# Performance work log

Measured on AMD Instinct MI355X. Metric: run time of the kernel, lower is better.

## Reference

```python
import jax, jax.numpy as jnp
import numpy as np
from functools import partial

C = 10   # number of regular-repr fields
G = 4    # C4 rotation group order
EPS = 1e-5


def _lift_kernel(w):
    """Lifting (trivial->regular) P4 kernel. w: [C, Cin, k, k] ->
    full kernel [C*G, Cin, k, k] with output channel layout (field, orientation)."""
    ks = [jnp.rot90(w, r, axes=(-2, -1)) for r in range(G)]  # each [C,Cin,k,k]
    k = jnp.stack(ks, axis=1)                                 # [C,G,Cin,k,k]
    return k.reshape(w.shape[0] * G, w.shape[1], w.shape[2], w.shape[3])


def _gconv_kernel(w):
    """Regular->regular P4 kernel. w: [Cout, Cin, G, k, k] (indexed by relative
    input orientation) -> full kernel [Cout*G, Cin*G, k, k].
    K[co*G+r, ci*G+s] = rot90(w[co, ci, (s-r) mod G], r)."""
    Cout, Cin, _, k1, k2 = w.shape
    ks = []
    for r in range(G):
        wr = jnp.roll(w, shift=r, axis=2)             # wr[..., s, :, :] = w[..., (s-r)%G]
        wr = jnp.rot90(wr, r, axes=(-2, -1))          # rotate spatially by r*90deg
        ks.append(wr)
    k = jnp.stack(ks, axis=1)                          # [Cout, G, Cin, G, k, k]
    return k.reshape(Cout * G, Cin * G, k1, k2)


def _conv(x, k, pad):
    return jax.lax.conv_general_dilated(
        x, k, window_strides=(1, 1), padding=pad,
        dimension_numbers=('NCHW', 'OIHW', 'NCHW'))


def _bn_relu(x, gamma, beta):
    """InnerBatchNorm (stats shared over the G orientations of each field) + ReLU."""
    B, CG, H, W = x.shape
    xr = x.reshape(B, C, G, H, W)
    m = xr.mean(axis=(0, 2, 3, 4), keepdims=True)
    v = xr.var(axis=(0, 2, 3, 4), keepdims=True)
    g = gamma[None, :, None, None, None]
    b = beta[None, :, None, None, None]
    y = (xr - m) * jax.lax.rsqrt(v + EPS) * g + b
    return jnp.maximum(y.reshape(B, CG, H, W), 0.0)


def _maxpool2(x):
    return jax.lax.reduce_window(x, -jnp.inf, jax.lax.max,
                                 (1, 1, 2, 2), (1, 1, 2, 2), 'VALID')


def setup_inputs() -> dict:
    key = jax.random.key(0)
    ks = jax.random.split(key, 20)
    B = 1024
    x = jax.random.normal(ks[0], (B, 1, 28, 28), dtype=jnp.float32)
    w1 = jax.random.normal(ks[1], (C, 1, 3, 3), dtype=jnp.float32) * 0.3
    w2 = jax.random.normal(ks[2], (C, C, G, 3, 3), dtype=jnp.float32) * 0.1
    w3 = jax.random.normal(ks[3], (C, C, G, 3, 3), dtype=jnp.float32) * 0.1
    w4 = jax.random.normal(ks[4], (C, C, G, 3, 3), dtype=jnp.float32) * 0.1
    w5 = jax.random.normal(ks[5], (C, C, G, 3, 3), dtype=jnp.float32) * 0.1
    w6 = jax.random.normal(ks[6], (C, C, G, 3, 3), dtype=jnp.float32) * 0.1
    w7 = jax.random.normal(ks[7], (C, C, G, 4, 4), dtype=jnp.float32) * 0.1
    g1 = jnp.ones((C,), jnp.float32) + 0.1 * jax.random.normal(ks[8], (C,))
    b1 = 0.1 * jax.random.normal(ks[9], (C,))
    g2 = jnp.ones((C,), jnp.float32) + 0.1 * jax.random.normal(ks[10], (C,))
    b2 = 0.1 * jax.random.normal(ks[11], (C,))
    gs = jnp.ones((C,), jnp.float32) + 0.1 * jax.random.normal(ks[12], (C,))
    bs = 0.1 * jax.random.normal(ks[13], (C,))
    wfc = jax.random.normal(ks[14], (10, C * 11 * 11), dtype=jnp.float32) * 0.05
    bfc = jnp.zeros((10,), jnp.float32)
    return dict(x=x, w1=w1, w2=w2, w3=w3, w4=w4, w5=w5, w6=w6, w7=w7,
                g1=g1, b1=b1, g2=g2, b2=b2, gs=gs, bs=bs, wfc=wfc, bfc=bfc)


PAD1 = [(1, 1), (1, 1)]
PAD0 = [(0, 0), (0, 0)]


def reference(x, w1, w2, w3, w4, w5, w6, w7, g1, b1, g2, b2, gs, bs, wfc, bfc):
    # block1: lifting P4 conv 3x3 pad1 + InnerBN + ReLU  -> [B, 40, 28, 28]
    h = _bn_relu(_conv(x, _lift_kernel(w1), PAD1), g1, b1)
    # block2: P4 conv + BN + ReLU + 2x2 max pool         -> [B, 40, 14, 14]
    h = _maxpool2(_bn_relu(_conv(h, _gconv_kernel(w2), PAD1), g2, b2))
    # blocks 3-6: P4 conv + shared BN/ReLU               -> [B, 40, 14, 14]
    for w in (w3, w4, w5, w6):
        h = _bn_relu(_conv(h, _gconv_kernel(w), PAD1), gs, bs)
    # block7: P4 conv 4x4 pad0 + shared BN/ReLU          -> [B, 40, 11, 11]
    h = _bn_relu(_conv(h, _gconv_kernel(w7), PAD0), gs, bs)
    # group pooling: max over the G orientations of each field -> [B, 10, 11, 11]
    B = h.shape[0]
    h = h.reshape(B, C, G, 11, 11).max(axis=2)
    # fc
    return h.reshape(B, -1) @ wfc.T + bfc
```

## Files before the change

### kernel.cpp

```cpp
#include <hip/hip_runtime.h>

#define EPSV 1e-5f
#define INV28 (1.f / 3211264.f)
#define INV14 (1.f / 802816.f)
#define INV11 (1.f / 495616.f)

typedef _Float16 v8h __attribute__((ext_vector_type(8)));
typedef _Float16 v4h __attribute__((ext_vector_type(4)));
typedef _Float16 v2h __attribute__((ext_vector_type(2)));
typedef float v4f __attribute__((ext_vector_type(4)));

__device__ __forceinline__ int h2i(v2h v) { union { v2h h; int i; } u; u.h = v; return u.i; }
__device__ __forceinline__ v2h i2h(int i) { union { v2h h; int i; } u; u.i = i; return u.h; }
__device__ __forceinline__ int pmax2(int a, int b) {
  v2h x = i2h(a), y = i2h(b), r;
  r[0] = x[0] > y[0] ? x[0] : y[0];
  r[1] = x[1] > y[1] ? x[1] : y[1];
  return h2i(r);
}

__device__ __forceinline__ int rotsrc(int r, int dy, int dx, int K) {
  int sy, sx;
  if (r == 0)      { sy = dy;       sx = dx; }
  else if (r == 1) { sy = dx;       sx = K - 1 - dy; }
  else if (r == 2) { sy = K - 1 - dy; sx = K - 1 - dx; }
  else             { sy = K - 1 - dx; sx = dy; }
  return sy * K + sx;
}

__device__ __forceinline__ float gw_val(const float* __restrict__ w, int oc, int g,
                                        int j, int KS) {
  int tap = g / 5, cig = g % 5, ci = cig * 8 + j;
  int co = oc >> 2, r = oc & 3, cin = ci >> 2, s = ci & 3;
  int srel = (s - r) & 3;
  return w[((co * 10 + cin) * 4 + srel) * (KS * KS) + rotsrc(r, tap / KS, tap % KS, KS)];
}

__device__ __forceinline__ float stat8a(const float* __restrict__ p, int i) {
  float v = 0.f;
#pragma unroll
  for (int c = 0; c < 8; ++c)
    v += __hip_atomic_load(&p[c * 32 + i], __ATOMIC_RELAXED, __HIP_MEMORY_SCOPE_AGENT);
  return v;
}

__global__ void prep_kernel(const float* __restrict__ w1, const float* __restrict__ w2,
                            const float* __restrict__ w3, const float* __restrict__ w4,
                            const float* __restrict__ w5, const float* __restrict__ w6,
                            const float* __restrict__ w7,
                            _Float16* __restrict__ K1h, _Float16* __restrict__ Wh,
                            float* __restrict__ stats) {
  int idx = blockIdx.x * blockDim.x + threadIdx.x;
  if (idx < 1792) { stats[idx] = 0.f; return; }
  idx -= 1792;
  if (idx < 1536) {
    int mt = idx >> 9, l = (idx >> 3) & 63, j = idx & 7;
    int m = l & 15, quad = l >> 4;
    int k = quad * 8 + j, oc = mt * 16 + m;
    float val = 0.f;
    if (k < 9 && oc < 40) {
      int c = oc >> 2, r = oc & 3;
      val = w1[c * 9 + rotsrc(r, k / 3, k % 3, 3)];
    }
    K1h[idx] = (_Float16)val;
    return;
  }
  idx -= 1536;
  if (idx < 92160) {
    int l = idx / 18432, r0 = idx % 18432;
    const float* w = (l == 0) ? w2 : (l == 1) ? w3 : (l == 2) ? w4 : (l == 3) ? w5 : w6;
    int mt = r0 / 6144, r1 = r0 % 6144;
    int c = r1 / 512, r2 = r1 % 512;
    int q = r2 / 128, r3 = r2 % 128;
    int ocl = r3 / 8, j = r3 % 8;
    int oc = mt * 16 + ocl, g = c * 4 + q;
    float val = 0.f;
    if (oc < 40 && g < 45) val = gw_val(w, oc, g, j, 3);
    Wh[idx] = (_Float16)val;
    return;
  }
  idx -= 92160;
  if (idx < 30720) {
    int mt = idx / 10240, r1 = idx % 10240;
    int c = r1 / 512, r2 = r1 % 512;
    int q = r2 / 128, r3 = r2 % 128;
    int ocl = r3 / 8, j = r3 % 8;
    int oc = mt * 16 + ocl, g = c * 4 + q;
    float val = 0.f;
    if (oc < 40) val = gw_val(w7, oc, g, j, 4);
    Wh[92160 + idx] = (_Float16)val;
  }
}

__global__ __launch_bounds__(256) void conv1_stats(
    const float* __restrict__ x, const _Float16* __restrict__ K1h,
    float* __restrict__ stats) {
  __shared__ float ximg[900];
  __shared__ float sstat[20];
  const int tid = threadIdx.x, img = blockIdx.x;
  if (tid < 20) sstat[tid] = 0.f;
  for (int i = tid; i < 900; i += 256) {
    int gy = i / 30 - 1, gx = i % 30 - 1;
    ximg[i] = (gy >= 0 && gy < 28 && gx >= 0 && gx < 28)
                  ? x[img * 784 + gy * 28 + gx] : 0.f;
  }
  __syncthreads();
  const int lane = tid & 63, wv = tid >> 6;
  const int m = lane & 15, quad = lane >> 4;
  v8h a1[3];
#pragma unroll
  for (int mt = 0; mt < 3; ++mt)
    a1[mt] = *(const v8h*)(K1h + (mt * 64 + lane) * 8);
  float s[3] = {0.f, 0.f, 0.f}, q[3] = {0.f, 0.f, 0.f};
  for (int st = wv; st < 49; st += 4) {
    const int p = st * 16 + m;
    const int y = p / 28, xx = p % 28;
    v8h b;
#pragma unroll
    for (int j = 0; j < 8; ++j) {
      const int t = quad * 8 + j;
      float v = 0.f;
      if (t < 9) v = ximg[(y + t / 3) * 30 + xx + t % 3];
      b[j] = (_Float16)v;
    }
#pragma unroll
    for (int mt = 0; mt < 3; ++mt) {
      v4f acc = {0.f, 0.f, 0.f, 0.f};
      acc = __builtin_amdgcn_mfma_f32_16x16x32_f16(a1[mt], b, acc, 0, 0, 0);
#pragma unroll
      for (int r = 0; r < 4; ++r) { float v = acc[r]; s[mt] += v; q[mt] += v * v; }
    }
  }
#pragma unroll
  for (int mt = 0; mt < 3; ++mt) {
    float sv = s[mt], qv = q[mt];
#pragma unroll
    for (int off = 1; off <= 8; off <<= 1) {
      sv += __shfl_xor(sv, off, 64);
      qv += __shfl_xor(qv, off, 64);
    }
    if (m == 0 && ((mt < 2) || (quad < 2))) {
      atomicAdd(&sstat[mt * 4 + quad], sv);
      atomicAdd(&sstat[10 + mt * 4 + quad], qv);
    }
  }
  __syncthreads();
  if (tid < 20) atomicAdd(&stats[(img & 7) * 32 + tid], sstat[tid]);
}

template<int R>
__device__ __forceinline__ void band_impl(
    const int img, const int y0,
    const float* __restrict__ x, const _Float16* __restrict__ K1h,
    const _Float16* __restrict__ Wl,
    float* __restrict__ xpatch, _Float16* __restrict__ tile,
    const float* __restrict__ sc, const float* __restrict__ sh,
    float* __restrict__ sstat, _Float16* __restrict__ T0) {
  constexpr int NPIX = R * 28, NSUB = NPIX / 16, NSW = (NSUB + 3) / 4;
  constexpr int SROWS = R + 2, XR = R + 4;
  const int tid = threadIdx.x;
  const int lane = tid & 63, wv = tid >> 6;
  const int m = lane & 15, quad = lane >> 4;

  for (int i = tid; i < XR * 32; i += 256) {
    int gy = y0 - 2 + i / 32, gx = i % 32 - 2;
    xpatch[i] = (gy >= 0 && gy < 28 && gx >= 0 && gx < 28)
                    ? x[(long)img * 784 + gy * 28 + gx] : 0.f;
  }
  __syncthreads();

  {
    v8h a1[3];
#pragma unroll
    for (int mt = 0; mt < 3; ++mt)
      a1[mt] = *(const v8h*)(K1h + (mt * 64 + lane) * 8);
    constexpr int NPIXS = SROWS * 30;
    constexpr int NST = (NPIXS + 15) / 16;
    for (int st = wv; st < NST; st += 4) {
      const int p = st * 16 + m;
      const int pc = p < NPIXS ? p : NPIXS - 1;
      const int iy = pc / 30, ix = pc % 30;
      v8h b;
#pragma unroll
      for (int j = 0; j < 8; ++j) {
        const int t = quad * 8 + j;
        float v = 0.f;
        if (t < 9) v = xpatch[(iy + t / 3) * 32 + ix + t % 3];
        b[j] = (_Float16)v;
      }
      const int gy = y0 + iy - 1, gx = ix - 1;
      const bool wr = p < NPIXS;
      const bool inb = wr && gy >= 0 && gy < 28 && gx >= 0 && gx < 28;
      _Float16* tb = &tile[pc * 40];
#pragma unroll
      for (int mt = 0; mt < 3; ++mt) {
        v4f a = {0.f, 0.f, 0.f, 0.f};
        a = __builtin_amdgcn_mfma_f32_16x16x32_f16(a1[mt], b, a, 0, 0, 0);
        if (((mt < 2) || (quad < 2)) && wr) {
          const int f = mt * 4 + quad;
          const float scf = sc[f], shf = sh[f];
          v4h pk;
#pragma unroll
          for (int r = 0; r < 4; ++r)
            pk[r] = inb ? (_Float16)fmaxf(0.f, fmaf(a[r], scf, shf)) : (_Float16)0.f;
          *(v4h*)(tb + mt * 16 + quad * 4) = pk;
        }
      }
    }
  }
  __syncthreads();

  int pbase[NSW];
  bool sv[NSW];
#pragma unroll
  for (int s = 0; s < NSW; ++s) {
    int ns = wv + 4 * s;
    sv[s] = ns < NSUB;
    int i = (sv[s] ? ns : 0) * 16 + m;
    int q = i >> 2, c2 = i & 3;
    int yy = 2 * (q / 14) + (c2 >> 1), xx = 2 * (q % 14) + (c2 & 1);
    pbase[s] = (yy * 30 + xx) * 40;
  }
  v4f acc[3][NSW] = {};

  const _Float16* wlane = Wl + (quad * 16 + m) * 8;
  for (int c = 0; c < 12; ++c) {
    int g = 4 * c + quad; g = g > 44 ? 44 : g;
    int tap = g / 5, cig = g - tap * 5;
    int boff = ((tap / 3) * 30 + (tap % 3)) * 40 + cig * 8;
    v8h bfr[NSW];
#pragma unroll
    for (int s = 0; s < NSW; ++s)
      if (sv[s]) bfr[s] = *(const v8h*)&tile[pbase[s] + boff];
    v8h afr[3];
#pragma unroll
    for (int mt = 0; mt < 3; ++mt)
      afr[mt] = *(const v8h*)(wlane + (mt * 12 + c) * 512);
#pragma unroll
    for (int s = 0; s < NSW; ++s)
      if (sv[s]) {
#pragma unroll
        for (int mt = 0; mt < 3; ++mt)
          acc[mt][s] = __builtin_amdgcn_mfma_f32_16x16x32_f16(afr[mt], bfr[s],
                                                             acc[mt][s], 0, 0, 0);
      }
  }

#pragma unroll
  for (int mt = 0; mt < 3; ++mt) {
    float svv = 0.f, qvv = 0.f;
#pragma unroll
    for (int s = 0; s < NSW; ++s)
      if (sv[s]) {
#pragma unroll
        for (int r = 0; r < 4; ++r) { float v = acc[mt][s][r]; svv += v; qvv += v * v; }
      }
    const bool ocok = (mt < 2) || (quad < 2);
#pragma unroll
    for (int off = 1; off <= 8; off <<= 1) {
      svv += __shfl_xor(svv, off, 64);
      qvv += __shfl_xor(qvv, off, 64);
    }
    if (m == 0 && ocok) {
      atomicAdd(&sstat[mt * 4 + quad], svv);
      atomicAdd(&sstat[10 + mt * 4 + quad], qvv);
    }
  }

#pragma unroll
  for (int s = 0; s < NSW; ++s) {
    if (!sv[s]) continue;
    const int ns = wv + 4 * s;
    const int q = ns * 4 + (m >> 2);
    const int tb4 = (img * 256 + (y0 / 2 + q / 14 + 1) * 16 + (q % 14 + 1)) * 40;
#pragma unroll
    for (int mt = 0; mt < 3; ++mt) {
      const bool ocok = (mt < 2) || (quad < 2);
      if (!ocok) continue;
      v2h w0, w1;
      w0[0] = (_Float16)acc[mt][s][0]; w0[1] = (_Float16)acc[mt][s][1];
      w1[0] = (_Float16)acc[mt][s][2]; w1[1] = (_Float16)acc[mt][s][3];
      int a0 = h2i(w0), a1 = h2i(w1);
      a0 = pmax2(a0, __shfl_xor(a0, 1, 64));
      a0 = pmax2(a0, __shfl_xor(a0, 2, 64));
      a1 = pmax2(a1, __shfl_xor(a1, 1, 64));
      a1 = pmax2(a1, __shfl_xor(a1, 2, 64));
      if ((m & 3) == 0) {
        v2h r0 = i2h(a0), r1 = i2h(a1);
        v4h o;
        o[0] = r0[0]; o[1] = r0[1]; o[2] = r1[0]; o[3] = r1[1];
        *(v4h*)(T0 + (long)tb4 + mt * 16 + quad * 4) = o;
      }
    }
  }
}

__global__ __launch_bounds__(256) void conv_band_all(
    const float* __restrict__ x, const _Float16* __restrict__ K1h,
    const _Float16* __restrict__ Wl, const float* __restrict__ pstats,
    const float* __restrict__ pgamma, const float* __restrict__ pbeta,
    _Float16* __restrict__ T0, float* __restrict__ stats) {
  __shared__ __attribute__((aligned(16))) _Float16 tile[10 * 30 * 40];
  __shared__ float xpatch[12 * 32];
  __shared__ float sc[10], sh[10], sstat[20];
  const int tid = threadIdx.x;
  if (tid < 20) sstat[tid] = 0.f;
  if (tid >= 32 && tid < 42) {
    int f = tid - 32;
    float mu = stat8a(pstats, f) * INV28, q = stat8a(pstats, 10 + f) * INV28;
    float isd = rsqrtf(q - mu * mu + EPSV);
    float s = pgamma[f] * isd;
    sc[f] = s; sh[f] = pbeta[f] - mu * s;
  }
  const int bid = blockIdx.x;
  int img;
  if (bid < 3072) {
    img = bid / 3;
    band_impl<8>(img, (bid % 3) * 8, x, K1h, Wl, xpatch, tile, sc, sh, sstat, T0);
  } else {
    img = bid - 3072;
    band_impl<4>(img, 24, x, K1h, Wl, xpatch, tile, sc, sh, sstat, T0);
  }
  __syncthreads();
  if (tid < 20) atomicAdd(&stats[(img & 7) * 32 + tid], sstat[tid]);
}

__global__ __launch_bounds__(256) void conv_tile(
    const _Float16* __restrict__ Tin, const _Float16* __restrict__ Wl,
    const float* __restrict__ pstats, const float* __restrict__ pg,
    const float* __restrict__ pb, float pinvn,
    _Float16* __restrict__ Tout, float* __restrict__ stG) {
  __shared__ __attribute__((aligned(16))) _Float16 tile[256 * 40];
  __shared__ v2h scH[10], shH[10];
  __shared__ float sstat[20];
  const int tid = threadIdx.x, img = blockIdx.x;
  const int lane = tid & 63, wv = tid >> 6;
  const int m = lane & 15, quad = lane >> 4;
  if (tid < 20) sstat[tid] = 0.f;
  if (tid >= 32 && tid < 42) {
    int f = tid - 32;
    float mu = stat8a(pstats, f) * pinvn, q = stat8a(pstats, 10 + f) * pinvn;
    float isd = rsqrtf(q - mu * mu + EPSV);
    float s = pg[f] * isd;
    _Float16 sH = (_Float16)s, hH = (_Float16)(pb[f] - mu * s);
    v2h t0, t1;
    t0[0] = sH; t0[1] = sH; t1[0] = hH; t1[1] = hH;
    scH[f] = t0; shH[f] = t1;
  }
  __syncthreads();
  {
    const int iy = tid >> 4, ix = tid & 15;
    const bool border = (iy == 0) | (iy == 15) | (ix == 0) | (ix == 15);
    const _Float16* src = Tin + ((long)img * 256 + tid) * 40;
    _Float16* dst = &tile[tid * 40];
    if (!border) {
#pragma unroll
      for (int cg5 = 0; cg5 < 5; ++cg5) {
        v8h rv = *(const v8h*)(src + cg5 * 8);
        v2h* r2 = (v2h*)&rv;
        v8h pk; v2h* p2 = (v2h*)&pk;
#pragma unroll
        for (int pr = 0; pr < 4; ++pr) {
          const int f = cg5 * 2 + (pr >> 1);
          v2h t = r2[pr] * scH[f] + shH[f];
          v2h o;
          o[0] = t[0] > (_Float16)0.f ? t[0] : (_Float16)0.f;
          o[1] = t[1] > (_Float16)0.f ? t[1] : (_Float16)0.f;
          p2[pr] = o;
        }
        *(v8h*)(dst + cg5 * 8) = pk;
      }
    } else {
      v8h z;
#pragma unroll
      for (int u = 0; u < 8; ++u) z[u] = (_Float16)0.f;
#pragma unroll
      for (int cg5 = 0; cg5 < 5; ++cg5) *(v8h*)(dst + cg5 * 8) = z;
    }
  }
  __syncthreads();

  int pb3[4], n3[4];
  bool sv3[4], va3[4];
#pragma unroll
  for (int s = 0; s < 4; ++s) {
    int ns = wv + 4 * s;
    sv3[s] = ns < 13;
    int n = ns * 16 + m;
    va3[s] = sv3[s] && (n < 196);
    n = n < 196 ? n : 195;
    n3[s] = n;
    pb3[s] = ((n / 14) * 16 + (n % 14)) * 40;
  }
  const int wofs = (quad * 16 + m) * 8;
  v4f acc[3][4];
#pragma unroll
  for (int mt = 0; mt < 3; ++mt)
#pragma unroll
    for (int s = 0; s < 4; ++s) acc[mt][s] = (v4f){0.f, 0.f, 0.f, 0.f};
  for (int c = 0; c < 12; ++c) {
    int g = 4 * c + quad; g = g > 44 ? 44 : g;
    int tap = g / 5, cig = g - tap * 5;
    int boff = ((tap / 3) * 16 + (tap % 3)) * 40 + cig * 8;
    v8h bfr[4];
#pragma unroll
    for (int s = 0; s < 4; ++s)
      if (sv3[s]) bfr[s] = *(const v8h*)&tile[pb3[s] + boff];
    v8h afr[3];
#pragma unroll
    for (int mt = 0; mt < 3; ++mt)
      afr[mt] = *(const v8h*)(Wl + wofs + (mt * 12 + c) * 512);
#pragma unroll
    for (int s = 0; s < 4; ++s)
      if (sv3[s]) {
#pragma unroll
        for (int mt = 0; mt < 3; ++mt)
          acc[mt][s] = __builtin_amdgcn_mfma_f32_16x16x32_f16(afr[mt], bfr[s],
                                                             acc[mt][s], 0, 0, 0);
      }
  }

#pragma unroll
  for (int mt = 0; mt < 3; ++mt) {
    float svv = 0.f, qvv = 0.f;
#pragma unroll
    for (int s = 0; s < 4; ++s)
      if (va3[s]) {
#pragma unroll
        for (int r = 0; r < 4; ++r) { float v = acc[mt][s][r]; svv += v; qvv += v * v; }
      }
    const bool ocok = (mt < 2) || (quad < 2);
#pragma unroll
    for (int off = 1; off <= 8; off <<= 1) {
      svv += __shfl_xor(svv, off, 64);
      qvv += __shfl_xor(qvv, off, 64);
    }
    if (m == 0 && ocok) {
      atomicAdd(&sstat[mt * 4 + quad], svv);
      atomicAdd(&sstat[10 + mt * 4 + quad], qvv);
    }
  }
  __syncthreads();
  if (tid < 20) atomicAdd(&stG[(img & 7) * 32 + tid], sstat[tid]);

#pragma unroll
  for (int mt = 0; mt < 3; ++mt) {
    const bool ocok = (mt < 2) || (quad < 2);
    if (!ocok) continue;
#pragma unroll
    for (int s = 0; s < 4; ++s)
      if (va3[s]) {
        v4h pk;
#pragma unroll
        for (int r = 0; r < 4; ++r) pk[r] = (_Float16)acc[mt][s][r];
        const int n = n3[s];
        *(v4h*)(Tout + ((long)img * 256 + (n / 14 + 1) * 16 + (n % 14 + 1)) * 40
                + mt * 16 + quad * 4) = pk;
      }
  }
}

__global__ __launch_bounds__(256) void conv7_tile(
    const _Float16* __restrict__ Tin, const _Float16* __restrict__ Wl,
    const float* __restrict__ pstats, const float* __restrict__ pg,
    const float* __restrict__ pb,
    _Float16* __restrict__ T7, float* __restrict__ stG) {
  __shared__ __attribute__((aligned(16))) _Float16 tile[256 * 40];
  __shared__ v2h scH[10], shH[10];
  __shared__ float sstat[20];
  const int tid = threadIdx.x, img = blockIdx.x;
  const int lane = tid & 63, wv = tid >> 6;
  const int m = lane & 15, quad = lane >> 4;
  if (tid < 20) sstat[tid] = 0.f;
  if (tid >= 32 && tid < 42) {
    int f = tid - 32;
    float mu = stat8a(pstats, f) * INV14, q = stat8a(pstats, 10 + f) * INV14;
    float isd = rsqrtf(q - mu * mu + EPSV);
    float s = pg[f] * isd;
    _Float16 sH = (_Float16)s, hH = (_Float16)(pb[f] - mu * s);
    v2h t0, t1;
    t0[0] = sH; t0[1] = sH; t1[0] = hH; t1[1] = hH;
    scH[f] = t0; shH[f] = t1;
  }
  __syncthreads();
  {
    const int iy = tid >> 4, ix = tid & 15;
    const bool border = (iy == 0) | (iy == 15) | (ix == 0) | (ix == 15);
    const _Float16* src = Tin + ((long)img * 256 + tid) * 40;
    _Float16* dst = &tile[tid * 40];
    if (!border) {
#pragma unroll
      for (int cg5 = 0; cg5 < 5; ++cg5) {
        v8h rv = *(const v8h*)(src + cg5 * 8);
        v2h* r2 = (v2h*)&rv;
        v8h pk; v2h* p2 = (v2h*)&pk;
#pragma unroll
        for (int pr = 0; pr < 4; ++pr) {
          const int f = cg5 * 2 + (pr >> 1);
          v2h t = r2[pr] * scH[f] + shH[f];
          v2h o;
          o[0] = t[0] > (_Float16)0.f ? t[0] : (_Float16)0.f;
          o[1] = t[1] > (_Float16)0.f ? t[1] : (_Float16)0.f;
          p2[pr] = o;
        }
        *(v8h*)(dst + cg5 * 8) = pk;
      }
    } else {
      v8h z;
#pragma unroll
      for (int u = 0; u < 8; ++u) z[u] = (_Float16)0.f;
#pragma unroll
      for (int cg5 = 0; cg5 < 5; ++cg5) *(v8h*)(dst + cg5 * 8) = z;
    }
  }
  __syncthreads();

  int pb7[2], n7[2];
  bool va7[2];
#pragma unroll
  for (int s = 0; s < 2; ++s) {
    int ns = wv + 4 * s;
    int n = ns * 16 + m;
    va7[s] = n < 121;
    n = n < 121 ? n : 120;
    n7[s] = n;
    pb7[s] = ((n / 11 + 1) * 16 + (n % 11 + 1)) * 40;
  }
  const int wofs = (quad * 16 + m) * 8;
  v4f acc[3][2];
#pragma unroll
  for (int mt = 0; mt < 3; ++mt)
#pragma unroll
    for (int s = 0; s < 2; ++s) acc[mt][s] = (v4f){0.f, 0.f, 0.f, 0.f};
  for (int c = 0; c < 20; ++c) {
    int g = 4 * c + quad;
    int tap = g / 5, cig = g - tap * 5;
    int boff = ((tap >> 2) * 16 + (tap & 3)) * 40 + cig * 8;
    v8h bfr[2];
#pragma unroll
    for (int s = 0; s < 2; ++s) bfr[s] = *(const v8h*)&tile[pb7[s] + boff];
    v8h afr[3];
#pragma unroll
    for (int mt = 0; mt < 3; ++mt)
      afr[mt] = *(const v8h*)(Wl + wofs + (mt * 20 + c) * 512);
#pragma unroll
    for (int s = 0; s < 2; ++s)
#pragma unroll
      for (int mt = 0; mt < 3; ++mt)
        acc[mt][s] = __builtin_amdgcn_mfma_f32_16x16x32_f16(afr[mt], bfr[s],
                                                           acc[mt][s], 0, 0, 0);
  }

#pragma unroll
  for (int mt = 0; mt < 3; ++mt) {
    float svv = 0.f, qvv = 0.f;
#pragma unroll
    for (int s = 0; s < 2; ++s)
      if (va7[s]) {
#pragma unroll
        for (int r = 0; r < 4; ++r) { float v = acc[mt][s][r]; svv += v; qvv += v * v; }
      }
    const bool ocok = (mt < 2) || (quad < 2);
#pragma unroll
    for (int off = 1; off <= 8; off <<= 1) {
      svv += __shfl_xor(svv, off, 64);
      qvv += __shfl_xor(qvv, off, 64);
    }
    if (m == 0 && ocok) {
      atomicAdd(&sstat[mt * 4 + quad], svv);
      atomicAdd(&sstat[10 + mt * 4 + quad], qvv);
    }
  }
  __syncthreads();
  if (tid < 20) atomicAdd(&stG[(img & 7) * 32 + tid], sstat[tid]);

#pragma unroll
  for (int mt = 0; mt < 3; ++mt) {
    const bool ocok = (mt < 2) || (quad < 2);
    if (!ocok) continue;
#pragma unroll
    for (int s = 0; s < 2; ++s)
      if (va7[s]) {
        v4h pk;
#pragma unroll
        for (int r = 0; r < 4; ++r) pk[r] = (_Float16)acc[mt][s][r];
        *(v4h*)(T7 + ((long)img * 121 + n7[s]) * 40 + mt * 16 + quad * 4) = pk;
      }
  }
}

__global__ __launch_bounds__(256) void head_kernel(
    const _Float16* __restrict__ T7, const float* __restrict__ stats7,
    const float* __restrict__ gs, const float* __restrict__ bs,
    const float* __restrict__ wfc, const float* __restrict__ bfc,
    float* __restrict__ out) {
  __shared__ float sc[10], sh[10];
  __shared__ float mbuf[1210];
  __shared__ float red[40];
  const int tid = threadIdx.x, img = blockIdx.x;
  if (tid < 10) {
    float mu = stat8a(stats7, tid) * INV11, q = stat8a(stats7, 10 + tid) * INV11;
    float isd = rsqrtf(q - mu * mu + EPSV);
    float s = gs[tid] * isd;
    sc[tid] = s;
    sh[tid] = bs[tid] - mu * s;
  }
  __syncthreads();
  for (int p = tid; p < 121; p += 256) {
    const _Float16* rp = T7 + ((long)img * 121 + p) * 40;
#pragma unroll
    for (int cg5 = 0; cg5 < 5; ++cg5) {
      v8h v = *(const v8h*)(rp + cg5 * 8);
#pragma unroll
      for (int fh = 0; fh < 2; ++fh) {
        const int f = cg5 * 2 + fh;
        float mx = fmaf((float)v[fh * 4], sc[f], sh[f]);
#pragma unroll
        for (int r = 1; r < 4; ++r)
          mx = fmaxf(mx, fmaf((float)v[fh * 4 + r], sc[f], sh[f]));
        mbuf[f * 121 + p] = fmaxf(0.f, mx);
      }
    }
  }
  __syncthreads();
  const int wv = tid >> 6;
  for (int k = 0; k < 10; ++k) {
    float p = 0.f;
    for (int j = tid; j < 1210; j += 256) p = fmaf(mbuf[j], wfc[k * 1210 + j], p);
#pragma unroll
    for (int off = 32; off > 0; off >>= 1) p += __shfl_xor(p, off, 64);
    if ((tid & 63) == 0) red[k * 4 + wv] = p;
  }
  __syncthreads();
  if (tid < 10)
    out[img * 10 + tid] = bfc[tid] + red[tid * 4] + red[tid * 4 + 1] +
                          red[tid * 4 + 2] + red[tid * 4 + 3];
}

extern "C" void kernel_launch(void* const* d_in, const int* in_sizes, int n_in,
                              void* d_out, int out_size, void* d_ws, size_t ws_size,
                              hipStream_t stream) {
  const float* x   = (const float*)d_in[0];
  const float* w1  = (const float*)d_in[1];
  const float* w2  = (const float*)d_in[2];
  const float* w3  = (const float*)d_in[3];
  const float* w4  = (const float*)d_in[4];
  const float* w5  = (const float*)d_in[5];
  const float* w6  = (const float*)d_in[6];
  const float* w7  = (const float*)d_in[7];
  const float* g1  = (const float*)d_in[8];
  const float* b1  = (const float*)d_in[9];
  const float* g2  = (const float*)d_in[10];
  const float* b2  = (const float*)d_in[11];
  const float* gs  = (const float*)d_in[12];
  const float* bs  = (const float*)d_in[13];
  const float* wfc = (const float*)d_in[14];
  const float* bfc = (const float*)d_in[15];

  float* ws = (float*)d_ws;
  float* stats  = ws;
  _Float16* K1h = (_Float16*)(ws + 1792);
  _Float16* Wh  = (_Float16*)(ws + 2560);
  _Float16* T0  = (_Float16*)(ws + 64000);
  _Float16* T1  = (_Float16*)(ws + 5306880L);
  _Float16* T7  = (_Float16*)(ws + 10549760L);

  prep_kernel<<<493, 256, 0, stream>>>(w1, w2, w3, w4, w5, w6, w7, K1h, Wh, stats);
  conv1_stats<<<1024, 256, 0, stream>>>(x, K1h, stats);
  conv_band_all<<<4096, 256, 0, stream>>>(x, K1h, Wh, stats, g1, b1, T0,
                                          stats + 256);
  conv_tile<<<1024, 256, 0, stream>>>(T0, Wh + 18432, stats + 256, g2, b2, INV28,
                                      T1, stats + 512);
  conv_tile<<<1024, 256, 0, stream>>>(T1, Wh + 36864, stats + 512, gs, bs, INV14,
                                      T0, stats + 768);
  conv_tile<<<1024, 256, 0, stream>>>(T0, Wh + 55296, stats + 768, gs, bs, INV14,
                                      T1, stats + 1024);
  conv_tile<<<1024, 256, 0, stream>>>(T1, Wh + 73728, stats + 1024, gs, bs, INV14,
                                      T0, stats + 1280);
  conv7_tile<<<1024, 256, 0, stream>>>(T0, Wh + 92160, stats + 1280, gs, bs,
                                       T7, stats + 1536);
  head_kernel<<<1024, 256, 0, stream>>>(T7, stats + 1536, gs, bs, wfc, bfc,
                                        (float*)d_out);
}
```

Before: 265.3 us.

## Fuse tail conv layers and head into one persistent kernel with grid barriers

Replaces the four conv_tile launches, conv7_tile and head_kernel with a single kernel where each block keeps one image's activations resident in LDS across layers. A spin-wait grid barrier on a global counter synchronises the cross-block batch-norm statistics between layers. This removes the global-memory round trips of intermediate activations and the per-launch overhead. It relies on all 1024 blocks being co-resident (launch_bounds 256,4). The BN+ReLU is now applied in fp32 instead of packed fp16, and the barrier has a spin-count timeout that could silently break correctness if blocks are not co-resident.

```diff
diff --git a/kernel.cpp b/kernel.cpp
--- a/kernel.cpp
+++ b/kernel.cpp
@@ -44,6 +44,19 @@
   return v;
 }
 
+__device__ __forceinline__ void grid_barrier(int* bar, int target) {
+  __syncthreads();
+  if (threadIdx.x == 0) {
+    __hip_atomic_fetch_add(bar, 1, __ATOMIC_ACQ_REL, __HIP_MEMORY_SCOPE_AGENT);
+    int spins = 0;
+    while (__hip_atomic_load(bar, __ATOMIC_ACQUIRE, __HIP_MEMORY_SCOPE_AGENT) < target) {
+      __builtin_amdgcn_s_sleep(8);
+      if (++spins > (1 << 19)) break;
+    }
+  }
+  __syncthreads();
+}
+
 __global__ void prep_kernel(const float* __restrict__ w1, const float* __restrict__ w2,
                             const float* __restrict__ w3, const float* __restrict__ w4,
                             const float* __restrict__ w5, const float* __restrict__ w6,
@@ -51,8 +64,8 @@
                             _Float16* __restrict__ K1h, _Float16* __restrict__ Wh,
                             float* __restrict__ stats) {
   int idx = blockIdx.x * blockDim.x + threadIdx.x;
-  if (idx < 1792) { stats[idx] = 0.f; return; }
-  idx -= 1792;
+  if (idx < 1800) { stats[idx] = 0.f; return; }
+  idx -= 1800;
   if (idx < 1536) {
     int mt = idx >> 9, l = (idx >> 3) & 63, j = idx & 7;
     int m = l & 15, quad = l >> 4;
@@ -325,48 +338,43 @@
   if (tid < 20) atomicAdd(&stats[(img & 7) * 32 + tid], sstat[tid]);
 }
 
-__global__ __launch_bounds__(256) void conv_tile(
-    const _Float16* __restrict__ Tin, const _Float16* __restrict__ Wl,
-    const float* __restrict__ pstats, const float* __restrict__ pg,
-    const float* __restrict__ pb, float pinvn,
-    _Float16* __restrict__ Tout, float* __restrict__ stG) {
+__global__ __launch_bounds__(256, 4) void tail_fused(
+    const _Float16* __restrict__ T0, const _Float16* __restrict__ Wh,
+    float* __restrict__ stG, int* __restrict__ bar,
+    const float* __restrict__ g2, const float* __restrict__ b2,
+    const float* __restrict__ gs, const float* __restrict__ bs,
+    const float* __restrict__ wfc, const float* __restrict__ bfc,
+    float* __restrict__ out) {
   __shared__ __attribute__((aligned(16))) _Float16 tile[256 * 40];
-  __shared__ v2h scH[10], shH[10];
-  __shared__ float sstat[20];
+  __shared__ float sc[10], sh[10], sstat[20];
+  __shared__ float red[40];
   const int tid = threadIdx.x, img = blockIdx.x;
   const int lane = tid & 63, wv = tid >> 6;
   const int m = lane & 15, quad = lane >> 4;
+
   if (tid < 20) sstat[tid] = 0.f;
   if (tid >= 32 && tid < 42) {
     int f = tid - 32;
-    float mu = stat8a(pstats, f) * pinvn, q = stat8a(pstats, 10 + f) * pinvn;
+    float mu = stat8a(stG + 256, f) * INV28, q = stat8a(stG + 256, 10 + f) * INV28;
     float isd = rsqrtf(q - mu * mu + EPSV);
-    float s = pg[f] * isd;
-    _Float16 sH = (_Float16)s, hH = (_Float16)(pb[f] - mu * s);
-    v2h t0, t1;
-    t0[0] = sH; t0[1] = sH; t1[0] = hH; t1[1] = hH;
-    scH[f] = t0; shH[f] = t1;
+    float s = g2[f] * isd;
+    sc[f] = s; sh[f] = b2[f] - mu * s;
   }
   __syncthreads();
   {
     const int iy = tid >> 4, ix = tid & 15;
     const bool border = (iy == 0) | (iy == 15) | (ix == 0) | (ix == 15);
-    const _Float16* src = Tin + ((long)img * 256 + tid) * 40;
+    const _Float16* src = T0 + ((long)img * 256 + tid) * 40;
     _Float16* dst = &tile[tid * 40];
     if (!border) {
 #pragma unroll
       for (int cg5 = 0; cg5 < 5; ++cg5) {
         v8h rv = *(const v8h*)(src + cg5 * 8);
-        v2h* r2 = (v2h*)&rv;
-        v8h pk; v2h* p2 = (v2h*)&pk;
-#pragma unroll
-        for (int pr = 0; pr < 4; ++pr) {
-          const int f = cg5 * 2 + (pr >> 1);
-          v2h t = r2[pr] * scH[f] + shH[f];
-          v2h o;
-          o[0] = t[0] > (_Float16)0.f ? t[0] : (_Float16)0.f;
-          o[1] = t[1] > (_Float16)0.f ? t[1] : (_Float16)0.f;
-          p2[pr] = o;
+        v8h pk;
+#pragma unroll
+        for (int u = 0; u < 8; ++u) {
+          const int f = (cg5 * 8 + u) >> 2;
+          pk[u] = (_Float16)fmaxf(0.f, fmaf((float)rv[u], sc[f], sh[f]));
         }
         *(v8h*)(dst + cg5 * 8) = pk;
       }
@@ -393,127 +401,89 @@
     pb3[s] = ((n / 14) * 16 + (n % 14)) * 40;
   }
   const int wofs = (quad * 16 + m) * 8;
-  v4f acc[3][4];
-#pragma unroll
-  for (int mt = 0; mt < 3; ++mt)
-#pragma unroll
-    for (int s = 0; s < 4; ++s) acc[mt][s] = (v4f){0.f, 0.f, 0.f, 0.f};
-  for (int c = 0; c < 12; ++c) {
-    int g = 4 * c + quad; g = g > 44 ? 44 : g;
-    int tap = g / 5, cig = g - tap * 5;
-    int boff = ((tap / 3) * 16 + (tap % 3)) * 40 + cig * 8;
-    v8h bfr[4];
-#pragma unroll
-    for (int s = 0; s < 4; ++s)
-      if (sv3[s]) bfr[s] = *(const v8h*)&tile[pb3[s] + boff];
-    v8h afr[3];
+
+#pragma unroll 1
+  for (int L = 0; L < 4; ++L) {
+    const _Float16* Wl = Wh + 18432 * (L + 1);
+    v4f acc[3][4];
 #pragma unroll
     for (int mt = 0; mt < 3; ++mt)
-      afr[mt] = *(const v8h*)(Wl + wofs + (mt * 12 + c) * 512);
-#pragma unroll
-    for (int s = 0; s < 4; ++s)
-      if (sv3[s]) {
-#pragma unroll
-        for (int mt = 0; mt < 3; ++mt)
-          acc[mt][s] = __builtin_amdgcn_mfma_f32_16x16x32_f16(afr[mt], bfr[s],
-                                                             acc[mt][s], 0, 0, 0);
-      }
-  }
-
-#pragma unroll
-  for (int mt = 0; mt < 3; ++mt) {
-    float svv = 0.f, qvv = 0.f;
-#pragma unroll
-    for (int s = 0; s < 4; ++s)
-      if (va3[s]) {
-#pragma unroll
-        for (int r = 0; r < 4; ++r) { float v = acc[mt][s][r]; svv += v; qvv += v * v; }
-      }
-    const bool ocok = (mt < 2) || (quad < 2);
-#pragma unroll
-    for (int off = 1; off <= 8; off <<= 1) {
-      svv += __shfl_xor(svv, off, 64);
-      qvv += __shfl_xor(qvv, off, 64);
-    }
-    if (m == 0 && ocok) {
-      atomicAdd(&sstat[mt * 4 + quad], svv);
-      atomicAdd(&sstat[10 + mt * 4 + quad], qvv);
-    }
-  }
-  __syncthreads();
-  if (tid < 20) atomicAdd(&stG[(img & 7) * 32 + tid], sstat[tid]);
-
-#pragma unroll
-  for (int mt = 0; mt < 3; ++mt) {
-    const bool ocok = (mt < 2) || (quad < 2);
-    if (!ocok) continue;
-#pragma unroll
-    for (int s = 0; s < 4; ++s)
-      if (va3[s]) {
-        v4h pk;
-#pragma unroll
-        for (int r = 0; r < 4; ++r) pk[r] = (_Float16)acc[mt][s][r];
-        const int n = n3[s];
-        *(v4h*)(Tout + ((long)img * 256 + (n / 14 + 1) * 16 + (n % 14 + 1)) * 40
-                + mt * 16 + quad * 4) = pk;
-      }
-  }
-}
-
-__global__ __launch_bounds__(256) void conv7_tile(
-    const _Float16* __restrict__ Tin, const _Float16* __restrict__ Wl,
-    const float* __restrict__ pstats, const float* __restrict__ pg,
-    const float* __restrict__ pb,
-    _Float16* __restrict__ T7, float* __restrict__ stG) {
-  __shared__ __attribute__((aligned(16))) _Float16 tile[256 * 40];
-  __shared__ v2h scH[10], shH[10];
-  __shared__ float sstat[20];
-  const int tid = threadIdx.x, img = blockIdx.x;
-  const int lane = tid & 63, wv = tid >> 6;
-  const int m = lane & 15, quad = lane >> 4;
-  if (tid < 20) sstat[tid] = 0.f;
-  if (tid >= 32 && tid < 42) {
-    int f = tid - 32;
-    float mu = stat8a(pstats, f) * INV14, q = stat8a(pstats, 10 + f) * INV14;
-    float isd = rsqrtf(q - mu * mu + EPSV);
-    float s = pg[f] * isd;
-    _Float16 sH = (_Float16)s, hH = (_Float16)(pb[f] - mu * s);
-    v2h t0, t1;
-    t0[0] = sH; t0[1] = sH; t1[0] = hH; t1[1] = hH;
-    scH[f] = t0; shH[f] = t1;
-  }
-  __syncthreads();
-  {
-    const int iy = tid >> 4, ix = tid & 15;
-    const bool border = (iy == 0) | (iy == 15) | (ix == 0) | (ix == 15);
-    const _Float16* src = Tin + ((long)img * 256 + tid) * 40;
-    _Float16* dst = &tile[tid * 40];
-    if (!border) {
-#pragma unroll
-      for (int cg5 = 0; cg5 < 5; ++cg5) {
-        v8h rv = *(const v8h*)(src + cg5 * 8);
-        v2h* r2 = (v2h*)&rv;
-        v8h pk; v2h* p2 = (v2h*)&pk;
-#pragma unroll
-        for (int pr = 0; pr < 4; ++pr) {
-          const int f = cg5 * 2 + (pr >> 1);
-          v2h t = r2[pr] * scH[f] + shH[f];
-          v2h o;
-          o[0] = t[0] > (_Float16)0.f ? t[0] : (_Float16)0.f;
-          o[1] = t[1] > (_Float16)0.f ? t[1] : (_Float16)0.f;
-          p2[pr] = o;
+#pragma unroll
+      for (int s = 0; s < 4; ++s) acc[mt][s] = (v4f){0.f, 0.f, 0.f, 0.f};
+    for (int c = 0; c < 12; ++c) {
+      int g = 4 * c + quad; g = g > 44 ? 44 : g;
+      int tap = g / 5, cig = g - tap * 5;
+      int boff = ((tap / 3) * 16 + (tap % 3)) * 40 + cig * 8;
+      v8h bfr[4];
+#pragma unroll
+      for (int s = 0; s < 4; ++s)
+        if (sv3[s]) bfr[s] = *(const v8h*)&tile[pb3[s] + boff];
+      v8h afr[3];
+#pragma unroll
+      for (int mt = 0; mt < 3; ++mt)
+        afr[mt] = *(const v8h*)(Wl + wofs + (mt * 12 + c) * 512);
+#pragma unroll
+      for (int s = 0; s < 4; ++s)
+        if (sv3[s]) {
+#pragma unroll
+          for (int mt = 0; mt < 3; ++mt)
+            acc[mt][s] = __builtin_amdgcn_mfma_f32_16x16x32_f16(afr[mt], bfr[s],
+                                                               acc[mt][s], 0, 0, 0);
         }
-        *(v8h*)(dst + cg5 * 8) = pk;
-      }
-    } else {
-      v8h z;
-#pragma unroll
-      for (int u = 0; u < 8; ++u) z[u] = (_Float16)0.f;
-#pragma unroll
-      for (int cg5 = 0; cg5 < 5; ++cg5) *(v8h*)(dst + cg5 * 8) = z;
-    }
-  }
-  __syncthreads();
+    }
+
+#pragma unroll
+    for (int mt = 0; mt < 3; ++mt) {
+      float svv = 0.f, qvv = 0.f;
+#pragma unroll
+      for (int s = 0; s < 4; ++s)
+        if (va3[s]) {
+#pragma unroll
+          for (int r = 0; r < 4; ++r) { float v = acc[mt][s][r]; svv += v; qvv += v * v; }
+        }
+      const bool ocok = (mt < 2) || (quad < 2);
+#pragma unroll
+      for (int off = 1; off <= 8; off <<= 1) {
+        svv += __shfl_xor(svv, off, 64);
+        qvv += __shfl_xor(qvv, off, 64);
+      }
+      if (m == 0 && ocok) {
+        atomicAdd(&sstat[mt * 4 + quad], svv);
+        atomicAdd(&sstat[10 + mt * 4 + quad], qvv);
+      }
+    }
+    __syncthreads();
+    if (tid < 20) atomicAdd(&stG[512 + 256 * L + (img & 7) * 32 + tid], sstat[tid]);
+    grid_barrier(bar, (L + 1) * 1024);
+
+    if (tid < 20) sstat[tid] = 0.f;
+    if (tid >= 32 && tid < 42) {
+      int f = tid - 32;
+      const float* ps = stG + 512 + 256 * L;
+      float mu = stat8a(ps, f) * INV14, q = stat8a(ps, 10 + f) * INV14;
+      float isd = rsqrtf(q - mu * mu + EPSV);
+      float s = gs[f] * isd;
+      sc[f] = s; sh[f] = bs[f] - mu * s;
+    }
+    __syncthreads();
+#pragma unroll
+    for (int mt = 0; mt < 3; ++mt) {
+      const bool ocok = (mt < 2) || (quad < 2);
+      if (!ocok) continue;
+      const float scf = sc[mt * 4 + quad], shf = sh[mt * 4 + quad];
+#pragma unroll
+      for (int s = 0; s < 4; ++s)
+        if (va3[s]) {
+          v4h pk;
+#pragma unroll
+          for (int r = 0; r < 4; ++r)
+            pk[r] = (_Float16)fmaxf(0.f, fmaf(acc[mt][s][r], scf, shf));
+          const int n = n3[s];
+          *(v4h*)(&tile[((n / 14 + 1) * 16 + (n % 14 + 1)) * 40 + mt * 16 + quad * 4]) = pk;
+        }
+    }
+    __syncthreads();
+  }
 
   int pb7[2], n7[2];
   bool va7[2];
@@ -526,31 +496,32 @@
     n7[s] = n;
     pb7[s] = ((n / 11 + 1) * 16 + (n % 11 + 1)) * 40;
   }
-  const int wofs = (quad * 16 + m) * 8;
-  v4f acc[3][2];
+  v4f acc7[3][2];
 #pragma unroll
   for (int mt = 0; mt < 3; ++mt)
 #pragma unroll
-    for (int s = 0; s < 2; ++s) acc[mt][s] = (v4f){0.f, 0.f, 0.f, 0.f};
-  for (int c = 0; c < 20; ++c) {
-    int g = 4 * c + quad;
-    int tap = g / 5, cig = g - tap * 5;
-    int boff = ((tap >> 2) * 16 + (tap & 3)) * 40 + cig * 8;
-    v8h bfr[2];
-#pragma unroll
-    for (int s = 0; s < 2; ++s) bfr[s] = *(const v8h*)&tile[pb7[s] + boff];
-    v8h afr[3];
-#pragma unroll
-    for (int mt = 0; mt < 3; ++mt)
-      afr[mt] = *(const v8h*)(Wl + wofs + (mt * 20 + c) * 512);
-#pragma unroll
-    for (int s = 0; s < 2; ++s)
+    for (int s = 0; s < 2; ++s) acc7[mt][s] = (v4f){0.f, 0.f, 0.f, 0.f};
+  {
+    const _Float16* Wl = Wh + 92160;
+    for (int c = 0; c < 20; ++c) {
+      int g = 4 * c + quad;
+      int tap = g / 5, cig = g - tap * 5;
+      int boff = ((tap >> 2) * 16 + (tap & 3)) * 40 + cig * 8;
+      v8h bfr[2];
+#pragma unroll
+      for (int s = 0; s < 2; ++s) bfr[s] = *(const v8h*)&tile[pb7[s] + boff];
+      v8h afr[3];
 #pragma unroll
       for (int mt = 0; mt < 3; ++mt)
-        acc[mt][s] = __builtin_amdgcn_mfma_f32_16x16x32_f16(afr[mt], bfr[s],
-                                                           acc[mt][s], 0, 0, 0);
-  }
-
+        afr[mt] = *(const v8h*)(Wl + wofs + (mt * 20 + c) * 512);
+#pragma unroll
+      for (int s = 0; s < 2; ++s)
+#pragma unroll
+        for (int mt = 0; mt < 3; ++mt)
+          acc7[mt][s] = __builtin_amdgcn_mfma_f32_16x16x32_f16(afr[mt], bfr[s],
+                                                              acc7[mt][s], 0, 0, 0);
+    }
+  }
 #pragma unroll
   for (int mt = 0; mt < 3; ++mt) {
     float svv = 0.f, qvv = 0.f;
@@ -558,7 +529,7 @@
     for (int s = 0; s < 2; ++s)
       if (va7[s]) {
 #pragma unroll
-        for (int r = 0; r < 4; ++r) { float v = acc[mt][s][r]; svv += v; qvv += v * v; }
+        for (int r = 0; r < 4; ++r) { float v = acc7[mt][s][r]; svv += v; qvv += v * v; }
       }
     const bool ocok = (mt < 2) || (quad < 2);
 #pragma unroll
@@ -572,58 +543,34 @@
     }
   }
   __syncthreads();
-  if (tid < 20) atomicAdd(&stG[(img & 7) * 32 + tid], sstat[tid]);
-
+  if (tid < 20) atomicAdd(&stG[1536 + (img & 7) * 32 + tid], sstat[tid]);
+  grid_barrier(bar, 5 * 1024);
+
+  float* mbuf = (float*)tile;
+  if (tid >= 32 && tid < 42) {
+    int f = tid - 32;
+    const float* ps = stG + 1536;
+    float mu = stat8a(ps, f) * INV11, q = stat8a(ps, 10 + f) * INV11;
+    float isd = rsqrtf(q - mu * mu + EPSV);
+    float s = gs[f] * isd;
+    sc[f] = s; sh[f] = bs[f] - mu * s;
+  }
+  __syncthreads();
 #pragma unroll
   for (int mt = 0; mt < 3; ++mt) {
     const bool ocok = (mt < 2) || (quad < 2);
     if (!ocok) continue;
+    const float scf = sc[mt * 4 + quad], shf = sh[mt * 4 + quad];
 #pragma unroll
     for (int s = 0; s < 2; ++s)
       if (va7[s]) {
-        v4h pk;
-#pragma unroll
-        for (int r = 0; r < 4; ++r) pk[r] = (_Float16)acc[mt][s][r];
-        *(v4h*)(T7 + ((long)img * 121 + n7[s]) * 40 + mt * 16 + quad * 4) = pk;
-      }
-  }
-}
-
-__global__ __launch_bounds__(256) void head_kernel(
-    const _Float16* __restrict__ T7, const float* __restrict__ stats7,
-    const float* __restrict__ gs, const float* __restrict__ bs,
-    const float* __restrict__ wfc, const float* __restrict__ bfc,
-    float* __restrict__ out) {
-  __shared__ float sc[10], sh[10];
-  __shared__ float mbuf[1210];
-  __shared__ float red[40];
-  const int tid = threadIdx.x, img = blockIdx.x;
-  if (tid < 10) {
-    float mu = stat8a(stats7, tid) * INV11, q = stat8a(stats7, 10 + tid) * INV11;
-    float isd = rsqrtf(q - mu * mu + EPSV);
-    float s = gs[tid] * isd;
-    sc[tid] = s;
-    sh[tid] = bs[tid] - mu * s;
-  }
-  __syncthreads();
-  for (int p = tid; p < 121; p += 256) {
-    const _Float16* rp = T7 + ((long)img * 121 + p) * 40;
-#pragma unroll
-    for (int cg5 = 0; cg5 < 5; ++cg5) {
-      v8h v = *(const v8h*)(rp + cg5 * 8);
-#pragma unroll
-      for (int fh = 0; fh < 2; ++fh) {
-        const int f = cg5 * 2 + fh;
-        float mx = fmaf((float)v[fh * 4], sc[f], sh[f]);
-#pragma unroll
-        for (int r = 1; r < 4; ++r)
-          mx = fmaxf(mx, fmaf((float)v[fh * 4 + r], sc[f], sh[f]));
-        mbuf[f * 121 + p] = fmaxf(0.f, mx);
-      }
-    }
-  }
-  __syncthreads();
-  const int wv = tid >> 6;
+        float mx = fmaf(acc7[mt][s][0], scf, shf);
+#pragma unroll
+        for (int r = 1; r < 4; ++r) mx = fmaxf(mx, fmaf(acc7[mt][s][r], scf, shf));
+        mbuf[(mt * 4 + quad) * 121 + n7[s]] = fmaxf(0.f, mx);
+      }
+  }
+  __syncthreads();
   for (int k = 0; k < 10; ++k) {
     float p = 0.f;
     for (int j = tid; j < 1210; j += 256) p = fmaf(mbuf[j], wfc[k * 1210 + j], p);
@@ -659,26 +606,15 @@
 
   float* ws = (float*)d_ws;
   float* stats  = ws;
-  _Float16* K1h = (_Float16*)(ws + 1792);
-  _Float16* Wh  = (_Float16*)(ws + 2560);
-  _Float16* T0  = (_Float16*)(ws + 64000);
-  _Float16* T1  = (_Float16*)(ws + 5306880L);
-  _Float16* T7  = (_Float16*)(ws + 10549760L);
-
-  prep_kernel<<<493, 256, 0, stream>>>(w1, w2, w3, w4, w5, w6, w7, K1h, Wh, stats);
+  int* bar      = (int*)(ws + 1792);
+  _Float16* K1h = (_Float16*)(ws + 1800);
+  _Float16* Wh  = (_Float16*)(ws + 2568);
+  _Float16* T0  = (_Float16*)(ws + 64008);
+
+  prep_kernel<<<494, 256, 0, stream>>>(w1, w2, w3, w4, w5, w6, w7, K1h, Wh, stats);
   conv1_stats<<<1024, 256, 0, stream>>>(x, K1h, stats);
   conv_band_all<<<4096, 256, 0, stream>>>(x, K1h, Wh, stats, g1, b1, T0,
                                           stats + 256);
-  conv_tile<<<1024, 256, 0, stream>>>(T0, Wh + 18432, stats + 256, g2, b2, INV28,
-                                      T1, stats + 512);
-  conv_tile<<<1024, 256, 0, stream>>>(T1, Wh + 36864, stats + 512, gs, bs, INV14,
-                                      T0, stats + 768);
-  conv_tile<<<1024, 256, 0, stream>>>(T0, Wh + 55296, stats + 768, gs, bs, INV14,
-                                      T1, stats + 1024);
-  conv_tile<<<1024, 256, 0, stream>>>(T1, Wh + 73728, stats + 1024, gs, bs, INV14,
-                                      T0, stats + 1280);
-  conv7_tile<<<1024, 256, 0, stream>>>(T0, Wh + 92160, stats + 1280, gs, bs,
-                                       T7, stats + 1536);
-  head_kernel<<<1024, 256, 0, stream>>>(T7, stats + 1536, gs, bs, wfc, bfc,
-                                        (float*)d_out);
-}
+  tail_fused<<<1024, 256, 0, stream>>>(T0, Wh, stats, bar, g2, b2, gs, bs,
+                                       wfc, bfc, (float*)d_out);
+}
```

After: 422.6 us. 59.3% more time.
